# Kernel tuning notes

Hardware: AMD Instinct MI355X
Metric: run time of the kernel (lower is better)

The kernel has to match this reference:

```python
import jax, jax.numpy as jnp
import numpy as np
import math

BS = 32; N_NODE = 400; N = BS * N_NODE; E = 204800
D = 200; HS = 1024; SEQ = 512
N_NTYPE = 4; N_ETYPE = 38
HEADS = 4; DPH = D // HEADS
K_LAYERS = 5
EP1 = 1.0


def _lin(key, fi, fo, lead=None):
    shape = (fi, fo) if lead is None else (lead, fi, fo)
    return jax.random.normal(key, shape, jnp.float32) * 0.05


def setup_inputs() -> dict:
    key = jax.random.key(0)
    ks = jax.random.split(key, 20)
    inp = {}
    inp['hidden_states'] = jax.random.normal(ks[0], (BS, SEQ, HS), jnp.float32)
    inp['X'] = jax.random.normal(ks[1], (N, D), jnp.float32)
    inp['node_feature_extra'] = jax.random.normal(ks[2], (N, D), jnp.float32)
    inp['edge_index'] = jax.random.randint(ks[3], (2, E), 0, N)
    inp['edge_type'] = jax.random.randint(ks[4], (E,), 0, N_ETYPE)
    inp['node_type'] = jax.random.randint(ks[5], (N,), 0, N_NTYPE)
    inp['epoch'] = 0
    edge_in = N_ETYPE + 1 + 2 * N_NTYPE  # one-hot edge type (+self-loop) + head/tail node-type one-hots
    inp['We1'] = _lin(ks[6], edge_in, D); inp['be1'] = jnp.zeros((D,), jnp.float32)
    inp['We2'] = _lin(ks[7], D, D);       inp['be2'] = jnp.zeros((D,), jnp.float32)
    inp['Wkey'] = _lin(ks[8], 3 * D, D, K_LAYERS);  inp['bkey'] = jnp.zeros((K_LAYERS, D), jnp.float32)
    inp['Wmsg'] = _lin(ks[9], 3 * D, D, K_LAYERS);  inp['bmsg'] = jnp.zeros((K_LAYERS, D), jnp.float32)
    inp['Wqry'] = _lin(ks[10], 2 * D, D, K_LAYERS); inp['bqry'] = jnp.zeros((K_LAYERS, D), jnp.float32)
    inp['Wm1'] = _lin(ks[11], D, D, K_LAYERS);      inp['bm1'] = jnp.zeros((K_LAYERS, D), jnp.float32)
    inp['Wm2'] = _lin(ks[12], D, D, K_LAYERS);      inp['bm2'] = jnp.zeros((K_LAYERS, D), jnp.float32)
    inp['Wq_att'] = _lin(ks[13], D, D); inp['bq_att'] = jnp.zeros((D,), jnp.float32)
    inp['Wk_att'] = _lin(ks[14], D, D); inp['bk_att'] = jnp.zeros((D,), jnp.float32)
    inp['Wv_att'] = _lin(ks[15], D, D); inp['bv_att'] = jnp.zeros((D,), jnp.float32)
    inp['Wproj'] = _lin(ks[16], HS, D); inp['bproj'] = jnp.zeros((D,), jnp.float32)
    return inp


def _segment_softmax(scores, seg, n):
    m = jax.ops.segment_max(scores, seg, num_segments=n)
    m = jnp.where(jnp.isfinite(m), m, 0.0)
    e = jnp.exp(scores - m[seg])
    s = jax.ops.segment_sum(e, seg, num_segments=n)
    return e / (s[seg] + 1e-16)


def _gat_layer(X, nfe, src, dst, edge_emb, Wk, bk, Wm, bm, Wq, bq, W1, b1, W2, b2):
    n = X.shape[0]
    x = jnp.concatenate([X, nfe], axis=1)            # [N, 2D]
    x_i = x[dst]; x_j = x[src]                       # [E', 2D]
    key = (jnp.concatenate([x_i, edge_emb], 1) @ Wk + bk).reshape(-1, HEADS, DPH)
    msg = (jnp.concatenate([x_j, edge_emb], 1) @ Wm + bm).reshape(-1, HEADS, DPH)
    qry = ((x_i @ Wq + bq).reshape(-1, HEADS, DPH)) / math.sqrt(DPH)
    scores = (qry * key).sum(-1)                     # [E', HEADS]
    alpha = _segment_softmax(scores, src, n)
    cnt = jax.ops.segment_sum(jnp.ones_like(alpha[:, 0]), src, num_segments=n)[src]
    alpha = alpha * cnt[:, None]                     # scale by src out-degree (QAGNN GATConvE)
    out_msg = (msg * alpha[..., None]).reshape(-1, D)
    aggr = jax.ops.segment_sum(out_msg, dst, num_segments=n)
    out = jax.nn.relu(aggr @ W1 + b1) @ W2 + b2      # MLP, BatchNorm(eval) ~ identity
    sensitivity = jnp.max(jnp.linalg.norm(out, axis=-1))
    return out, sensitivity


def _forward(hidden_states, X, node_feature_extra, edge_index, edge_type, node_type,
             We1, be1, We2, be2, Wkey, bkey, Wmsg, bmsg, Wqry, bqry, Wm1, bm1, Wm2, bm2,
             Wq_att, bq_att, Wk_att, bk_att, Wv_att, bv_att, Wproj, bproj):
    n = X.shape[0]
    # self loops with edge type n_etype, as in GATConvE
    loop = jnp.arange(n)
    src = jnp.concatenate([edge_index[0], loop])
    dst = jnp.concatenate([edge_index[1], loop])
    et = jnp.concatenate([edge_type, jnp.full((n,), N_ETYPE, edge_type.dtype)])
    edge_vec = jax.nn.one_hot(et, N_ETYPE + 1, dtype=X.dtype)
    hvec = jax.nn.one_hot(node_type[src], N_NTYPE, dtype=X.dtype)
    tvec = jax.nn.one_hot(node_type[dst], N_NTYPE, dtype=X.dtype)
    # shared edge encoder (same edges each layer -> hoisted, identical math)
    edge_emb = jax.nn.relu(jnp.concatenate([edge_vec, hvec, tvec], 1) @ We1 + be1) @ We2 + be2
    context = hidden_states[:, 0, :] @ Wproj + bproj  # [bs, D]
    K = (context @ Wk_att + bk_att)[:, None, :]       # [bs, 1, D]
    V = (context @ Wv_att + bv_att)[:, None, :]
    nkey = jax.random.key(123)
    _X = X
    for li in range(K_LAYERS):
        _X, sens = _gat_layer(_X, node_feature_extra, src, dst, edge_emb,
                              Wkey[li], bkey[li], Wmsg[li], bmsg[li], Wqry[li], bqry[li],
                              Wm1[li], bm1[li], Wm2[li], bm2[li])
        _X = jax.nn.gelu(_X, approximate=False)
        Xb = _X.reshape(BS, N_NODE, D)
        Q = Xb @ Wq_att + bq_att
        Q = Q / jnp.maximum(jnp.linalg.norm(Q, axis=-1, keepdims=True), 1e-12)
        att = jnp.einsum('bnd,bmd->bnm', Q, K) / math.sqrt(D)  # [bs, n_node, 1]
        scale = jax.lax.stop_gradient(sens / (EP1 / 4.0))      # Laplace DP noise (non-diff in orig)
        noise = scale * jax.random.laplace(jax.random.fold_in(nkey, li), att.shape, att.dtype)
        att = att + noise
        _X = jnp.einsum('bnm,bmd->bnd', att, V).reshape(-1, D)
    return _X


def reference(hidden_states, X, node_feature_extra, edge_index, edge_type, node_type, epoch,
              We1, be1, We2, be2, Wkey, bkey, Wmsg, bmsg, Wqry, bqry, Wm1, bm1, Wm2, bm2,
              Wq_att, bq_att, Wk_att, bk_att, Wv_att, bv_att, Wproj, bproj):
    return _forward(hidden_states, X, node_feature_extra, edge_index, edge_type, node_type,
                    We1, be1, We2, be2, Wkey, bkey, Wmsg, bmsg, Wqry, bqry, Wm1, bm1, Wm2, bm2,
                    Wq_att, bq_att, Wk_att, bk_att, Wv_att, bv_att, Wproj, bproj)
```

## Files before the change

kernel.cpp:

```cpp
#include <hip/hip_runtime.h>
#include <stdint.h>

#define NBATCH 32
#define NNODE  400
#define NN     12800
#define NE     204800
#define EPE    217600
#define DD     200
#define NETYPE 38
#define NCOMBO 624
#define HSZ    1024
#define SEQQ   512
#define NL     5
#define ACH    128

__device__ __forceinline__ unsigned short f2bf(float x){
  uint32_t u = __float_as_uint(x);
  uint32_t r = (u + 0x7fffu + ((u>>16)&1u)) >> 16;
  return (unsigned short)r;
}
__device__ __forceinline__ float bf2f(unsigned short b){
  return __uint_as_float(((uint32_t)b)<<16);
}

__device__ __forceinline__ uint32_t rotl32(uint32_t x, uint32_t d){ return (x<<d)|(x>>(32u-d)); }

__device__ void tf2x32(uint32_t k0, uint32_t k1, uint32_t x0, uint32_t x1,
                       uint32_t* o0, uint32_t* o1){
  uint32_t ks0=k0, ks1=k1, ks2=k0^k1^0x1BD11BDAu;
  uint32_t ks[3]={ks0,ks1,ks2};
  x0 += ks0; x1 += ks1;
  const uint32_t rotA[4]={13,15,26,6};
  const uint32_t rotB[4]={17,29,16,24};
  #pragma unroll
  for (int i=0;i<5;i++){
    const uint32_t* r = (i&1)? rotB : rotA;
    #pragma unroll
    for (int j=0;j<4;j++){ x0 += x1; x1 = rotl32(x1, r[j]); x1 ^= x0; }
    x0 += ks[(i+1)%3];
    x1 += ks[(i+2)%3] + (uint32_t)(i+1);
  }
  *o0=x0; *o1=x1;
}

__global__ void k_noise(float* noise){
  int i = blockIdx.x*256+threadIdx.x;
  if (i >= NL*NN) return;
  int l = i / NN, j = i % NN;
  uint32_t k0,k1,o0,o1,bits;
  tf2x32(0u,123u,0u,(uint32_t)l,&k0,&k1);
  tf2x32(k0,k1,0u,(uint32_t)j,&o0,&o1);
  bits = o0 ^ o1;
  uint32_t fb = (bits>>9) | 0x3f800000u;
  float f = __uint_as_float(fb) - 1.0f;
  const float minv = -0.99999994039535522461f;
  float u = fmaxf(minv, f*2.0f + minv);
  float s = (u>0.f)?1.f:((u<0.f)?-1.f:0.f);
  noise[i] = s*log1pf(-fabsf(u));
}

__global__ void k_edges(const int* eidx, int* outdeg, int* indeg){
  int e = blockIdx.x*256+threadIdx.x; if (e>=EPE) return;
  int s,dv;
  if (e < NE){ s = eidx[e]; dv = eidx[NE+e]; } else { s = dv = e-NE; }
  atomicAdd(&outdeg[s],1); atomicAdd(&indeg[dv],1);
}

__global__ void k_scan(const int* outdeg, const int* indeg, int* sstart, int* dstart){
  __shared__ int buf[2][1024];
  for (int which=0; which<2; ++which){
    const int* a = which? indeg : outdeg;
    int* o = which? dstart : sstart;
    int t = threadIdx.x;
    int c0 = t*13;
    int s = 0;
    for (int i=c0;i<c0+13;i++) if (i<NN) s += a[i];
    __syncthreads();
    buf[0][t]=s; __syncthreads();
    int cur=0;
    #pragma unroll
    for (int off=1; off<1024; off<<=1){
      int v = buf[cur][t];
      if (t>=off) v += buf[cur][t-off];
      buf[cur^1][t]=v; cur^=1; __syncthreads();
    }
    int run = buf[cur][t] - s;
    for (int i=c0;i<c0+13;i++) if (i<NN){ o[i]=run; run+=a[i]; }
    if (t==0) o[NN]=EPE;
  }
}

__global__ void k_scatter(const int* eidx, const int* etype, const int* ntype,
                          const int* sstart, const int* dstart, int* sfill, int* dfill,
                          int* s_dst, int* s_combo, int* d_src, int* d_combo, int* s_dpos){
  int e = blockIdx.x*256+threadIdx.x; if (e>=EPE) return;
  int s,dv,et;
  if (e<NE){ s=eidx[e]; dv=eidx[NE+e]; et=etype[e]; } else { s=dv=e-NE; et=NETYPE; }
  int c = et*16 + ntype[s]*4 + ntype[dv];
  int p = sstart[s] + atomicAdd(&sfill[s],1);
  s_dst[p]=dv; s_combo[p]=c;
  int q = dstart[dv] + atomicAdd(&dfill[dv],1);
  d_src[q]=s; d_combo[q]=c; s_dpos[p]=q;
}

__global__ void k_ehid(const float* We1, const float* be1, float* ehid){
  int i = blockIdx.x*256+threadIdx.x; if (i>=NCOMBO*DD) return;
  int c = i/DD, d = i%DD;
  int et=c>>4, ht=(c>>2)&3, tt=c&3;
  float v = We1[et*DD+d] + We1[(39+ht)*DD+d] + We1[(43+tt)*DD+d] + be1[d];
  ehid[i] = fmaxf(v,0.f);
}

__global__ void k_cvt_xcat(const float* X, const float* nfe, unsigned short* xbf){
  int i=blockIdx.x*256+threadIdx.x; if (i>=NN*448) return;
  int n=i/448, d=i%448;
  float v = (d<200)? X[(size_t)n*200+d] : (d<400)? nfe[(size_t)n*200+(d-200)] : 0.f;
  xbf[i] = f2bf(v);
}
__global__ void k_cvt_nfe(const float* nfe, unsigned short* nbf){
  int i=blockIdx.x*256+threadIdx.x; if (i>=NN*224) return;
  int n=i/224, d=i%224;
  nbf[i] = (d<200)? f2bf(nfe[(size_t)n*200+d]) : 0;
}
__global__ void k_cvt_flat(const float* src, unsigned short* dst, int n){
  int i=blockIdx.x*256+threadIdx.x; if (i>=n) return;
  dst[i] = f2bf(src[i]);
}

struct WJob { const float* src; unsigned short* dst; int Ksrc; int Kpad; };
struct WArgs { WJob j[26]; };
__global__ void k_wswz(WArgs a){
  WJob jb = a.j[blockIdx.z];
  int i = blockIdx.x*256+threadIdx.x;
  if (i >= jb.Kpad*256) return;
  int k = i>>8, n = i&255;
  unsigned short v = 0;
  if (k<jb.Ksrc && n<200) v = f2bf(jb.src[(size_t)k*200+n]);
  jb.dst[(((size_t)(k>>3))*256 + n)*8 + (k&7)] = v;
}

typedef __attribute__((ext_vector_type(8))) short bf16x8;
typedef __attribute__((ext_vector_type(4))) float f32x4;

struct MJob { const unsigned short* A; const unsigned short* B; const float* bias;
              float* C; unsigned short* Cbf; const float* r1v; const float* r1m;
              int relu; float scale; int gelu; int cbfs; };
struct MArgs { int Kpad; MJob j[3]; };

__global__ __launch_bounds__(256) void k_mgemm(MArgs g){
  const MJob jb = g.j[blockIdx.z];
  const int lane = threadIdx.x&63, w = threadIdx.x>>6;
  const int lr = lane&15, lk = lane>>4;
  const int m0 = blockIdx.y*128 + w*32;
  const int n0 = blockIdx.x*64;
  const int Kp = g.Kpad;
  f32x4 acc[2][4] = {};
  const unsigned short* a0 = jb.A + (size_t)(m0+lr)*Kp + lk*8;
  const unsigned short* a1 = a0 + (size_t)16*Kp;
  for (int ks=0; ks<Kp; ks+=32){
    bf16x8 af0 = *(const bf16x8*)(a0 + ks);
    bf16x8 af1 = *(const bf16x8*)(a1 + ks);
    const unsigned short* bb = jb.B + (((size_t)(ks>>3) + lk)*256 + n0 + lr)*8;
    bf16x8 b0 = *(const bf16x8*)(bb);
    bf16x8 b1 = *(const bf16x8*)(bb + 128);
    bf16x8 b2 = *(const bf16x8*)(bb + 256);
    bf16x8 b3 = *(const bf16x8*)(bb + 384);
    acc[0][0]=__builtin_amdgcn_mfma_f32_16x16x32_bf16(af0,b0,acc[0][0],0,0,0);
    acc[0][1]=__builtin_amdgcn_mfma_f32_16x16x32_bf16(af0,b1,acc[0][1],0,0,0);
    acc[0][2]=__builtin_amdgcn_mfma_f32_16x16x32_bf16(af0,b2,acc[0][2],0,0,0);
    acc[0][3]=__builtin_amdgcn_mfma_f32_16x16x32_bf16(af0,b3,acc[0][3],0,0,0);
    acc[1][0]=__builtin_amdgcn_mfma_f32_16x16x32_bf16(af1,b0,acc[1][0],0,0,0);
    acc[1][1]=__builtin_amdgcn_mfma_f32_16x16x32_bf16(af1,b1,acc[1][1],0,0,0);
    acc[1][2]=__builtin_amdgcn_mfma_f32_16x16x32_bf16(af1,b2,acc[1][2],0,0,0);
    acc[1][3]=__builtin_amdgcn_mfma_f32_16x16x32_bf16(af1,b3,acc[1][3],0,0,0);
  }
  #pragma unroll
  for (int mt=0; mt<2; ++mt){
    int mbase = m0 + mt*16 + lk*4;
    #pragma unroll
    for (int nt=0; nt<4; ++nt){
      int n = n0 + nt*16 + lr;
      #pragma unroll
      for (int r=0;r<4;r++){
        int m = mbase + r;
        float v = acc[mt][nt][r];
        if (n < 200){
          if (jb.r1v)  v += jb.r1v[m]*jb.r1m[(size_t)(m/NNODE)*200 + n];
          if (jb.bias) v += jb.bias[n];
          v *= jb.scale;
          if (jb.relu) v = fmaxf(v, 0.f);
          if (jb.C)    jb.C[(size_t)m*200 + n] = v;
          if (jb.Cbf){
            float o = jb.gelu? 0.5f*v*(1.0f+erff(v*0.70710678118654752440f)) : v;
            jb.Cbf[(size_t)m*jb.cbfs + n] = f2bf(o);
          }
        } else if (jb.Cbf && jb.cbfs==224 && n < 224){
          jb.Cbf[(size_t)m*224 + n] = 0;
        }
      }
    }
  }
}

struct RJob { const float* A; const float* W; const float* bias; float* C; int K; size_t lda; };
struct RArgs { RJob j[12]; float* part; int NS; int Kc; };
__global__ __launch_bounds__(256) void k_rowpart(RArgs a){
  RJob jb = a.j[blockIdx.z];
  int m = blockIdx.x, s = blockIdx.y;
  int k0 = s*a.Kc, k1 = k0 + a.Kc; if (k1 > jb.K) k1 = jb.K;
  int kc = k1 - k0;
  __shared__ float row[128];
  const float* ap = jb.A + (size_t)m*jb.lda + k0;
  for (int k=threadIdx.x; k<kc; k+=256) row[k]=ap[k];
  __syncthreads();
  int n = threadIdx.x;
  if (n < 200){
    float acc = 0.f;
    const float* wp = jb.W + (size_t)k0*200 + n;
    for (int kk=0; kk<kc; ++kk) acc += row[kk]*wp[(size_t)kk*200];
    a.part[(((size_t)blockIdx.z*32 + m)*8 + s)*200 + n] = acc;
  }
}
__global__ __launch_bounds__(256) void k_rowred(RArgs a){
  RJob jb = a.j[blockIdx.z];
  int m = blockIdx.x, n = threadIdx.x;
  if (n >= 200) return;
  float acc = jb.bias? jb.bias[n] : 0.f;
  for (int s=0; s<a.NS; ++s) acc += a.part[(((size_t)blockIdx.z*32 + m)*8 + s)*200 + n];
  jb.C[(size_t)m*200+n] = acc;
}

struct Job {
  const float* A; const float* W; const float* bias; float* C;
  const float* r1v; const float* r1m; int relu;
};
struct GArgs { int M,N,K,lda; Job j[12]; };

#define BMT 64
#define BNT 64
#define BKT 16

__global__ __launch_bounds__(256) void k_gemm(GArgs g){
  const Job jb = g.j[blockIdx.z];
  const int m0 = blockIdx.y*BMT, n0 = blockIdx.x*BNT;
  __shared__ float As[BKT][BMT+4];
  __shared__ float Bs[BKT][BNT+4];
  float acc[4][4]={};
  const int t = threadIdx.x;
  const int tx = t & 15, ty = t >> 4;
  for (int k0=0; k0<g.K; k0+=BKT){
    {
      int r = t>>2, cq = t&3;
      int m = m0+r, k = k0+cq*4;
      float4 v = make_float4(0.f,0.f,0.f,0.f);
      if (m < g.M && k < g.K){
        if (k+3 < g.K) v = *(const float4*)(jb.A + (size_t)m*g.lda + k);
        else {
          const float* ap = jb.A + (size_t)m*g.lda;
          float tm[4]={0.f,0.f,0.f,0.f};
          for (int qq=0;qq<4;qq++) if (k+qq<g.K) tm[qq]=ap[k+qq];
          v = make_float4(tm[0],tm[1],tm[2],tm[3]);
        }
      }
      As[cq*4+0][r]=v.x; As[cq*4+1][r]=v.y; As[cq*4+2][r]=v.z; As[cq*4+3][r]=v.w;
    }
    {
      int r = t>>4, cq = t&15;
      int k = k0+r, n = n0+cq*4;
      float4 v = make_float4(0.f,0.f,0.f,0.f);
      if (k < g.K && n < g.N){
        if (n+3 < g.N) v = *(const float4*)(jb.W + (size_t)k*g.N + n);
        else { const float* wp = jb.W + (size_t)k*g.N;
          float tm[4]={0.f,0.f,0.f,0.f};
          for (int qq=0;qq<4;qq++) if (n+qq<g.N) tm[qq]=wp[n+qq];
          v = make_float4(tm[0],tm[1],tm[2],tm[3]); }
      }
      Bs[r][cq*4+0]=v.x; Bs[r][cq*4+1]=v.y; Bs[r][cq*4+2]=v.z; Bs[r][cq*4+3]=v.w;
    }
    __syncthreads();
    int kend = g.K-k0; if (kend>BKT) kend=BKT;
    for (int kk=0;kk<kend;kk++){
      float4 av = *(const float4*)&As[kk][ty*4];
      float4 bv = *(const float4*)&Bs[kk][tx*4];
      float a[4]={av.x,av.y,av.z,av.w};
      float b[4]={bv.x,bv.y,bv.z,bv.w};
      #pragma unroll
      for (int i=0;i<4;i++){
        #pragma unroll
        for (int jq=0;jq<4;jq++) acc[i][jq] += a[i]*b[jq];
      }
    }
    __syncthreads();
  }
  #pragma unroll
  for (int i=0;i<4;i++){
    int m = m0+ty*4+i; if (m>=g.M) continue;
    int bidx = m / NNODE;
    #pragma unroll
    for (int jq=0;jq<4;jq++){
      int n = n0+tx*4+jq; if (n>=g.N) continue;
      float v = acc[i][jq];
      if (jb.bias) v += jb.bias[n];
      if (jb.r1v)  v += jb.r1v[m]*jb.r1m[(size_t)bidx*g.N + n];
      if (jb.relu) v = fmaxf(v,0.f);
      jb.C[(size_t)m*g.N+n] = v;
    }
  }
}

__global__ void k_prep(const float* qv, const float* Ak, float* ps){
  int wid = threadIdx.x>>6, lane = threadIdx.x&63;
  int n = blockIdx.x*4 + wid; if (n>=NN) return;
  float acch[4]={0.f,0.f,0.f,0.f};
  for (int d=lane; d<DD; d+=64)
    acch[d/50] += qv[(size_t)n*DD+d]*Ak[(size_t)n*DD+d];
  for (int off=1; off<64; off<<=1){
    #pragma unroll
    for (int h=0;h<4;h++) acch[h] += __shfl_xor(acch[h], off);
  }
  if (lane==0){
    #pragma unroll
    for (int h=0;h<4;h++) ps[n*4+h]=acch[h];
  }
}

__global__ __launch_bounds__(256) void k_score(const int* s_dst, const int* s_combo, const float* qv,
                        const float* Bk, const float* ps, float* scores){
  int p = blockIdx.x*64 + (threadIdx.x>>2);
  if (p>=EPE) return;
  int sub = threadIdx.x&3;
  int dv = s_dst[p], c = s_combo[p];
  const float4* qr = (const float4*)(qv + (size_t)dv*DD);
  const float4* br = (const float4*)(Bk + (size_t)c*DD);
  float acc[4]={0.f,0.f,0.f,0.f};
  #pragma unroll
  for (int i=0;i<13;i++){
    int q = sub + 4*i;
    if (q < 50){
      float4 a = qr[q], b = br[q];
      int d = q*4;
      acc[(d+0)/50] += a.x*b.x;
      acc[(d+1)/50] += a.y*b.y;
      acc[(d+2)/50] += a.z*b.z;
      acc[(d+3)/50] += a.w*b.w;
    }
  }
  #pragma unroll
  for (int off=1; off<4; off<<=1){
    #pragma unroll
    for (int h=0;h<4;h++) acc[h] += __shfl_xor(acc[h], off);
  }
  scores[(size_t)p*4+sub] = ps[dv*4+sub] + acc[sub];
}

__global__ void k_softmax(const int* sstart, const int* s_dpos, const float* scores, float* alpha_d){
  int n = blockIdx.x;
  int st = sstart[n], en = sstart[n+1];
  int cnt = en-st;
  int t = threadIdx.x;
  float mx = -3.402823466e38f;
  for (int i=t; i<cnt*4; i+=64) mx = fmaxf(mx, scores[(size_t)(st+(i>>2))*4 + (i&3)]);
  for (int off=4; off<64; off<<=1) mx = fmaxf(mx, __shfl_xor(mx,off));
  float sm=0.f;
  for (int i=t; i<cnt*4; i+=64) sm += expf(scores[(size_t)(st+(i>>2))*4 + (i&3)] - mx);
  for (int off=4; off<64; off<<=1) sm += __shfl_xor(sm,off);
  float scale = (float)cnt / (sm + 1e-16f);
  for (int i=t; i<cnt*4; i+=64){
    int p = st+(i>>2), h = i&3;
    float a = expf(scores[(size_t)p*4+h]-mx)*scale;
    alpha_d[(size_t)s_dpos[p]*4+h] = a;
  }
}

__global__ __launch_bounds__(256) void k_aggr(const int* dstart, const int* d_src, const int* d_combo,
                       const float* alpha_d,
                       const unsigned short* Am, const unsigned short* Bm,
                       unsigned short* aggr_bf){
  __shared__ float red[4][200];
  __shared__ float s_al[ACH*4];
  __shared__ int   s_s[ACH], s_c[ACH];
  int v = blockIdx.x;
  int w = threadIdx.x>>6, lane = threadIdx.x&63;
  int st=dstart[v], en=dstart[v+1];
  float acc[8]={0.f,0.f,0.f,0.f,0.f,0.f,0.f,0.f};
  int h[8];
  #pragma unroll
  for (int j=0;j<8;j++) h[j] = (lane*8+j)/50;
  for (int c0=st; c0<en; c0+=ACH){
    int cnt = en-c0; if (cnt>ACH) cnt=ACH;
    __syncthreads();
    for (int i=threadIdx.x; i<cnt; i+=256){ s_s[i]=d_src[c0+i]; s_c[i]=d_combo[c0+i]; }
    for (int i=threadIdx.x; i<cnt*4; i+=256){ s_al[i]=alpha_d[(size_t)c0*4+i]; }
    __syncthreads();
    if (lane < 25){
      for (int q=w; q<cnt; q+=4){
        int s=s_s[q], c=s_c[q];
        bf16x8 am = *(const bf16x8*)(Am + (size_t)s*200 + lane*8);
        bf16x8 bm = *(const bf16x8*)(Bm + (size_t)c*200 + lane*8);
        #pragma unroll
        for (int j=0;j<8;j++){
          float a = s_al[q*4+h[j]];
          acc[j] += a*(bf2f((unsigned short)am[j]) + bf2f((unsigned short)bm[j]));
        }
      }
    }
  }
  if (lane < 25){
    #pragma unroll
    for (int j=0;j<8;j++) red[w][lane*8+j]=acc[j];
  }
  __syncthreads();
  int d = threadIdx.x;
  if (d < 200){
    float r = red[0][d]+red[1][d]+red[2][d]+red[3][d];
    aggr_bf[(size_t)v*224+d]=f2bf(r);
  } else if (d < 224){
    aggr_bf[(size_t)v*224+d]=0;
  }
}

__global__ void k_sens(const float* out, float* sens2, int l){
  __shared__ float smax[4];
  int wid = threadIdx.x>>6, lane = threadIdx.x&63;
  int gw = blockIdx.x*4 + wid;
  float mx = 0.f;
  for (int n = gw; n < NN; n += 256){
    const float4* row = (const float4*)(out + (size_t)n*DD);
    float ss = 0.f;
    if (lane < 50){ float4 v = row[lane]; ss = v.x*v.x + v.y*v.y + v.z*v.z + v.w*v.w; }
    for (int off=1; off<64; off<<=1) ss += __shfl_xor(ss, off);
    mx = fmaxf(mx, ss);
  }
  if (lane==0) smax[wid] = mx;
  __syncthreads();
  if (threadIdx.x==0){
    float m = fmaxf(fmaxf(smax[0],smax[1]),fmaxf(smax[2],smax[3]));
    atomicMax((int*)&sens2[l], __float_as_int(m));
  }
}

__global__ void k_att(const float* Q, const float* Katt, const float* Vatt,
                      const float* sens2, const float* noise, int l,
                      float* att, float* outX){
  int wid=threadIdx.x>>6, lane=threadIdx.x&63;
  int n=blockIdx.x*4+wid; if (n>=NN) return;
  int b=n/NNODE;
  float qq=0.f, qk=0.f;
  for (int d=lane; d<DD; d+=64){
    float q=Q[(size_t)n*DD+d];
    qq += q*q; qk += q*Katt[b*DD+d];
  }
  for (int off=1;off<64;off<<=1){ qq+=__shfl_xor(qq,off); qk+=__shfl_xor(qk,off); }
  float nrm = fmaxf(sqrtf(qq), 1e-12f);
  float a = (qk/nrm) * 0.07071067811865475244f;
  a += 4.0f*sqrtf(sens2[l]) * noise[(size_t)l*NN + n];
  if (lane==0) att[n]=a;
  if (outX){
    for (int d=lane; d<DD; d+=64) outX[(size_t)n*DD+d] = a*Vatt[b*DD+d];
  }
}

static inline Job mkjob(const float* A, const float* W, const float* bias, float* C,
                        const float* r1v, const float* r1m, int relu){
  Job j; j.A=A; j.W=W; j.bias=bias; j.C=C; j.r1v=r1v; j.r1m=r1m; j.relu=relu; return j;
}

static inline void gemm_launch(hipStream_t stream, int M,int N,int K,int lda,
                               const Job* jobs, int nj){
  GArgs g; g.M=M; g.N=N; g.K=K; g.lda=lda;
  for (int i=0;i<nj;i++) g.j[i]=jobs[i];
  for (int i=nj;i<12;i++) g.j[i]=jobs[0];
  dim3 grid((N+BNT-1)/BNT,(M+BMT-1)/BMT,nj);
  k_gemm<<<grid,256,0,stream>>>(g);
}

static inline RJob mkrjob(const float* A, const float* W, const float* bias, float* C,
                          int K, size_t lda){
  RJob j; j.A=A; j.W=W; j.bias=bias; j.C=C; j.K=K; j.lda=lda; return j;
}

static inline void rgemm_launch(hipStream_t stream, const RJob* jobs, int nj,
                                float* part, int NS, int Kc){
  RArgs a;
  for (int i=0;i<nj;i++) a.j[i]=jobs[i];
  for (int i=nj;i<12;i++) a.j[i]=jobs[0];
  a.part = part; a.NS = NS; a.Kc = Kc;
  k_rowpart<<<dim3(NBATCH,NS,nj),256,0,stream>>>(a);
  k_rowred <<<dim3(NBATCH,1,nj),256,0,stream>>>(a);
}

static inline MJob mkmjob(const unsigned short* A, const unsigned short* B, const float* bias,
                          float* C, unsigned short* Cbf, const float* r1v, const float* r1m,
                          int relu, float scale, int gelu, int cbfs){
  MJob j; j.A=A; j.B=B; j.bias=bias; j.C=C; j.Cbf=Cbf; j.r1v=r1v; j.r1m=r1m;
  j.relu=relu; j.scale=scale; j.gelu=gelu; j.cbfs=cbfs; return j;
}

static inline void mgemm_launch(hipStream_t stream, int Kpad, const MJob* jobs, int nj){
  MArgs a; a.Kpad=Kpad;
  for (int i=0;i<nj;i++) a.j[i]=jobs[i];
  for (int i=nj;i<3;i++) a.j[i]=jobs[0];
  k_mgemm<<<dim3(4,100,nj),256,0,stream>>>(a);
}

extern "C" void kernel_launch(void* const* d_in, const int* in_sizes, int n_in,
                              void* d_out, int out_size, void* d_ws, size_t ws_size,
                              hipStream_t stream){
  const float* hs    = (const float*)d_in[0];
  const float* X     = (const float*)d_in[1];
  const float* nfe   = (const float*)d_in[2];
  const int*   eidx  = (const int*)d_in[3];
  const int*   etype = (const int*)d_in[4];
  const int*   ntype = (const int*)d_in[5];
  const float* We1   = (const float*)d_in[7];
  const float* be1   = (const float*)d_in[8];
  const float* We2   = (const float*)d_in[9];
  const float* be2   = (const float*)d_in[10];
  const float* Wkey  = (const float*)d_in[11];
  const float* bkey  = (const float*)d_in[12];
  const float* Wmsg  = (const float*)d_in[13];
  const float* bmsg  = (const float*)d_in[14];
  const float* Wqry  = (const float*)d_in[15];
  const float* bqry  = (const float*)d_in[16];
  const float* Wm1   = (const float*)d_in[17];
  const float* bm1   = (const float*)d_in[18];
  const float* Wm2   = (const float*)d_in[19];
  const float* bm2   = (const float*)d_in[20];
  const float* Wq_att= (const float*)d_in[21];
  const float* bq_att= (const float*)d_in[22];
  const float* Wk_att= (const float*)d_in[23];
  const float* bk_att= (const float*)d_in[24];
  const float* Wv_att= (const float*)d_in[25];
  const float* bv_att= (const float*)d_in[26];
  const float* Wproj = (const float*)d_in[27];
  const float* bproj = (const float*)d_in[28];
  float* outp = (float*)d_out;

  char* cur = (char*)d_ws;
  auto allocf = [&](size_t n)->float*{ float* p=(float*)cur; cur += ((n*4+255)/256)*256; return p; };
  auto alloci = [&](size_t n)->int*  { int*   p=(int*)cur;   cur += ((n*4+255)/256)*256; return p; };
  auto allocb = [&](size_t n)->unsigned short*{ unsigned short* p=(unsigned short*)cur; cur += ((n*2+255)/256)*256; return p; };

  float* noise  = allocf((size_t)NL*NN);
  float* ehid   = allocf((size_t)NCOMBO*DD);
  float* eemb   = allocf((size_t)NCOMBO*DD);
  float* Bk     = allocf((size_t)NL*NCOMBO*DD);
  float* Bm     = allocf((size_t)NL*NCOMBO*DD);
  float* context= allocf((size_t)NBATCH*DD);
  float* Katt   = allocf((size_t)NBATCH*DD);
  float* Vatt   = allocf((size_t)NBATCH*DD);
  float* CKk    = allocf((size_t)4*NBATCH*DD);
  float* CKm    = allocf((size_t)4*NBATCH*DD);
  float* CKq    = allocf((size_t)4*NBATCH*DD);
  float* Ak     = allocf((size_t)NN*DD);
  float* Aq     = allocf((size_t)NN*DD);
  float* ps     = allocf((size_t)NN*4);
  float* scores = allocf((size_t)EPE*4);
  float* alphad = allocf((size_t)EPE*4);
  float* Q      = allocf((size_t)NN*DD);
  float* outb   = allocf((size_t)NN*DD);
  float* att    = allocf((size_t)NN);
  float* sens2  = allocf(8);
  float* rpart  = allocf((size_t)12*NBATCH*8*200);
  unsigned short* am_bf   = allocb((size_t)NN*200);
  unsigned short* bm_bf   = allocb((size_t)NL*NCOMBO*DD);
  unsigned short* xcat_bf = allocb((size_t)NN*448);
  unsigned short* nfe_bf  = allocb((size_t)NN*224);
  unsigned short* aggr_bf = allocb((size_t)NN*224);
  unsigned short* tmp1_bf = allocb((size_t)NN*224);
  unsigned short* gelu_bf = allocb((size_t)NN*224);
  unsigned short* wkx0  = allocb((size_t)448*256);
  unsigned short* wmx0  = allocb((size_t)448*256);
  unsigned short* wqx0  = allocb((size_t)448*256);
  unsigned short* wkN   = allocb((size_t)4*224*256);
  unsigned short* wmN   = allocb((size_t)4*224*256);
  unsigned short* wqN   = allocb((size_t)4*224*256);
  unsigned short* wm1s  = allocb((size_t)5*224*256);
  unsigned short* wm2s  = allocb((size_t)5*224*256);
  unsigned short* wqatts= allocb((size_t)224*256);
  int* sstart = alloci(NN+1);
  int* dstart = alloci(NN+1);
  int* outdeg = alloci(NN);
  int* indeg  = alloci(NN);
  int* sfill  = alloci(NN);
  int* dfill  = alloci(NN);
  int* s_dst  = alloci(EPE);
  int* s_combo= alloci(EPE);
  int* d_src  = alloci(EPE);
  int* d_combo= alloci(EPE);
  int* s_dpos = alloci(EPE);
  if ((size_t)(cur-(char*)d_ws) > ws_size) return;

  hipMemsetAsync(outdeg,0,(size_t)4*NN*4,stream);
  hipMemsetAsync(sens2 ,0,32,stream);

  k_noise<<<(NL*NN+255)/256,256,0,stream>>>(noise);
  k_edges<<<(EPE+255)/256,256,0,stream>>>(eidx,outdeg,indeg);
  k_scan<<<1,1024,0,stream>>>(outdeg,indeg,sstart,dstart);
  k_scatter<<<(EPE+255)/256,256,0,stream>>>(eidx,etype,ntype,sstart,dstart,sfill,dfill,
                                            s_dst,s_combo,d_src,d_combo,s_dpos);
  k_ehid<<<(NCOMBO*DD+255)/256,256,0,stream>>>(We1,be1,ehid);
  { Job j = mkjob(ehid,We2,be2,eemb,0,0,0); gemm_launch(stream,NCOMBO,DD,DD,DD,&j,1); }
  { Job js[10];
    for (int l=0;l<NL;l++){
      js[2*l+0]=mkjob(eemb, Wkey + (size_t)l*600*DD + 400*DD, 0, Bk + (size_t)l*NCOMBO*DD, 0,0,0);
      js[2*l+1]=mkjob(eemb, Wmsg + (size_t)l*600*DD + 400*DD, bmsg + (size_t)l*DD,
                      Bm + (size_t)l*NCOMBO*DD, 0,0,0);
    }
    gemm_launch(stream,NCOMBO,DD,DD,DD,js,10);
  }
  k_cvt_flat<<<(NL*NCOMBO*DD+255)/256,256,0,stream>>>(Bm, bm_bf, NL*NCOMBO*DD);
  k_cvt_xcat<<<(NN*448+255)/256,256,0,stream>>>(X,nfe,xcat_bf);
  k_cvt_nfe<<<(NN*224+255)/256,256,0,stream>>>(nfe,nfe_bf);
  { WArgs wa; int wn=0;
    auto addw=[&](const float* s, unsigned short* d, int Ks, int Kp){
      wa.j[wn].src=s; wa.j[wn].dst=d; wa.j[wn].Ksrc=Ks; wa.j[wn].Kpad=Kp; wn++; };
    addw(Wkey, wkx0, 400,448);
    addw(Wmsg, wmx0, 400,448);
    addw(Wqry, wqx0, 400,448);
    for (int l=1;l<NL;l++){
      addw(Wkey + (size_t)l*600*DD + 200*DD, wkN + (size_t)(l-1)*224*256, 200,224);
      addw(Wmsg + (size_t)l*600*DD + 200*DD, wmN + (size_t)(l-1)*224*256, 200,224);
      addw(Wqry + (size_t)l*400*DD + 200*DD, wqN + (size_t)(l-1)*224*256, 200,224);
    }
    for (int l=0;l<NL;l++){
      addw(Wm1 + (size_t)l*DD*DD, wm1s + (size_t)l*224*256, 200,224);
      addw(Wm2 + (size_t)l*DD*DD, wm2s + (size_t)l*224*256, 200,224);
    }
    addw(Wq_att, wqatts, 200,224);
    k_wswz<<<dim3(448,1,wn),256,0,stream>>>(wa);
  }
  { RJob j = mkrjob(hs, Wproj, bproj, context, HSZ, (size_t)SEQQ*HSZ);
    rgemm_launch(stream, &j, 1, rpart, 8, 128); }
  { RJob js[2] = { mkrjob(context, Wk_att, bk_att, Katt, DD, DD),
                   mkrjob(context, Wv_att, bv_att, Vatt, DD, DD) };
    rgemm_launch(stream, js, 2, rpart, 2, 100); }
  { RJob js[12];
    for (int l=1;l<NL;l++){
      js[3*(l-1)+0]=mkrjob(Vatt, Wkey + (size_t)l*600*DD, 0, CKk + (size_t)(l-1)*NBATCH*DD, DD, DD);
      js[3*(l-1)+1]=mkrjob(Vatt, Wmsg + (size_t)l*600*DD, 0, CKm + (size_t)(l-1)*NBATCH*DD, DD, DD);
      js[3*(l-1)+2]=mkrjob(Vatt, Wqry + (size_t)l*400*DD, 0, CKq + (size_t)(l-1)*NBATCH*DD, DD, DD);
    }
    rgemm_launch(stream, js, 12, rpart, 4, 50);
  }

  const float invs = 0.14142135623730950488f;
  for (int l=0;l<NL;l++){
    const float* bkey_l = bkey + (size_t)l*DD;
    const float* bqry_l = bqry + (size_t)l*DD;
    const float* Bk_l = Bk + (size_t)l*NCOMBO*DD;
    const unsigned short* Bm_l = bm_bf + (size_t)l*NCOMBO*DD;

    if (l==0){
      MJob js[3] = { mkmjob(xcat_bf, wkx0, bkey_l, Ak, 0,     0,0,0, 1.f,0, 224),
                     mkmjob(xcat_bf, wmx0, 0,      0,  am_bf, 0,0,0, 1.f,0, 200),
                     mkmjob(xcat_bf, wqx0, bqry_l, Aq, 0,     0,0,0, invs,0, 224) };
      mgemm_launch(stream,448,js,3);
    } else {
      const float* ckk = CKk + (size_t)(l-1)*NBATCH*DD;
      const float* ckm = CKm + (size_t)(l-1)*NBATCH*DD;
      const float* ckq = CKq + (size_t)(l-1)*NBATCH*DD;
      MJob js[3] = { mkmjob(nfe_bf, wkN + (size_t)(l-1)*224*256, bkey_l, Ak, 0,     att, ckk, 0, 1.f,0, 224),
                     mkmjob(nfe_bf, wmN + (size_t)(l-1)*224*256, 0,      0,  am_bf, att, ckm, 0, 1.f,0, 200),
                     mkmjob(nfe_bf, wqN + (size_t)(l-1)*224*256, bqry_l, Aq, 0,     att, ckq, 0, invs,0, 224) };
      mgemm_launch(stream,224,js,3);
    }
    k_prep<<<NN/4,256,0,stream>>>(Aq,Ak,ps);
    k_score<<<(EPE*4+255)/256,256,0,stream>>>(s_dst,s_combo,Aq,Bk_l,ps,scores);
    k_softmax<<<NN,64,0,stream>>>(sstart,s_dpos,scores,alphad);
    k_aggr<<<NN,256,0,stream>>>(dstart,d_src,d_combo,alphad,am_bf,Bm_l,aggr_bf);
    { MJob j = mkmjob(aggr_bf, wm1s + (size_t)l*224*256, bm1 + (size_t)l*DD, 0, tmp1_bf, 0,0,1, 1.f,0, 224);
      mgemm_launch(stream,224,&j,1); }
    { MJob j = mkmjob(tmp1_bf, wm2s + (size_t)l*224*256, bm2 + (size_t)l*DD, outb, gelu_bf, 0,0,0, 1.f,1, 224);
      mgemm_launch(stream,224,&j,1); }
    k_sens<<<64,256,0,stream>>>(outb,sens2,l);
    { MJob j = mkmjob(gelu_bf, wqatts, bq_att, Q, 0, 0,0,0, 1.f,0, 224);
      mgemm_launch(stream,224,&j,1); }
    k_att<<<NN/4,256,0,stream>>>(Q,Katt,Vatt,sens2,noise,l,att,(l==NL-1)? outp : (float*)0);
  }
}
```

Measured before the change: 1.119 ms.

## Fuse key/query/message GEMMs with per-head query-key dot product

Replaces the three-job batched GEMM plus the separate k_prep kernel with one kernel that computes key, query and message projections per 64-row block and reduces the query·key per-head dot products in registers. This removes the fp32 Ak buffer write and re-read, and drops a kernel launch. In exchange the grid shrinks to 200 blocks, each doing all three GEMMs serially over all 256 output columns with no LDS tiling, so there is less parallelism on the GPU and the A fragments are reloaded per pass.

```diff
diff --git a/kernel.cpp b/kernel.cpp
--- a/kernel.cpp
+++ b/kernel.cpp
@@ -141,6 +141,113 @@
 
 typedef __attribute__((ext_vector_type(8))) short bf16x8;
 typedef __attribute__((ext_vector_type(4))) float f32x4;
+
+struct M3Args {
+  const unsigned short* A; int Kp;
+  const unsigned short *wk, *wq, *wm;
+  const float *bkey, *bqry;
+  const float *att, *ckk, *ckq, *ckm;
+  float* qv; unsigned short* am; float* ps; float invs;
+};
+
+__device__ __forceinline__ void mm16(const unsigned short* a0, const unsigned short* W,
+                                     int Kp, int n0, int lk, int lr, f32x4 acc[4]){
+  for (int ks=0; ks<Kp; ks+=32){
+    bf16x8 af = *(const bf16x8*)(a0 + ks);
+    const unsigned short* bb = W + (((size_t)(ks>>3)+lk)*256 + n0 + lr)*8;
+    acc[0]=__builtin_amdgcn_mfma_f32_16x16x32_bf16(af, *(const bf16x8*)(bb      ), acc[0],0,0,0);
+    acc[1]=__builtin_amdgcn_mfma_f32_16x16x32_bf16(af, *(const bf16x8*)(bb + 128), acc[1],0,0,0);
+    acc[2]=__builtin_amdgcn_mfma_f32_16x16x32_bf16(af, *(const bf16x8*)(bb + 256), acc[2],0,0,0);
+    acc[3]=__builtin_amdgcn_mfma_f32_16x16x32_bf16(af, *(const bf16x8*)(bb + 384), acc[3],0,0,0);
+  }
+}
+
+__global__ __launch_bounds__(256) void k_mgemm3(M3Args g){
+  const int lane = threadIdx.x&63, w = threadIdx.x>>6;
+  const int lr = lane&15, lk = lane>>4;
+  const int mw = blockIdx.x*64 + w*16;
+  const int Kp = g.Kp;
+  const unsigned short* a0 = g.A + (size_t)(mw+lr)*Kp + lk*8;
+
+  int   mrow[4]; int bidx[4]; float attv[4];
+  #pragma unroll
+  for (int rr=0;rr<4;rr++){
+    mrow[rr] = mw + lk*4 + rr;
+    bidx[rr] = mrow[rr]/NNODE;
+    attv[rr] = g.att ? g.att[mrow[rr]] : 0.f;
+  }
+  float ps[4][4] = {};
+  float akv[4][4];
+
+  #pragma unroll
+  for (int ni=0; ni<4; ++ni){
+    const int n0 = ni*64;
+    {
+      f32x4 acc[4] = {};
+      mm16(a0, g.wk, Kp, n0, lk, lr, acc);
+      #pragma unroll
+      for (int nt=0;nt<4;nt++){
+        int d = n0 + nt*16 + lr;
+        bool ok = d < 200;
+        float bias = ok? g.bkey[d] : 0.f;
+        #pragma unroll
+        for (int rr=0;rr<4;rr++){
+          float v = acc[nt][rr] + bias;
+          if (g.att && ok) v += attv[rr]*g.ckk[(size_t)bidx[rr]*200 + d];
+          akv[nt][rr] = ok? v : 0.f;
+        }
+      }
+    }
+    {
+      f32x4 acc[4] = {};
+      mm16(a0, g.wq, Kp, n0, lk, lr, acc);
+      #pragma unroll
+      for (int nt=0;nt<4;nt++){
+        int d = n0 + nt*16 + lr;
+        bool ok = d < 200;
+        float bias = ok? g.bqry[d] : 0.f;
+        int hd = d/50;
+        #pragma unroll
+        for (int rr=0;rr<4;rr++){
+          float v = acc[nt][rr] + bias;
+          if (g.att && ok) v += attv[rr]*g.ckq[(size_t)bidx[rr]*200 + d];
+          v *= g.invs;
+          if (ok){
+            g.qv[(size_t)mrow[rr]*200 + d] = v;
+            float p = v*akv[nt][rr];
+            #pragma unroll
+            for (int h=0;h<4;h++) ps[rr][h] += (hd==h)? p : 0.f;
+          }
+        }
+      }
+    }
+    {
+      f32x4 acc[4] = {};
+      mm16(a0, g.wm, Kp, n0, lk, lr, acc);
+      #pragma unroll
+      for (int nt=0;nt<4;nt++){
+        int d = n0 + nt*16 + lr;
+        bool ok = d < 200;
+        #pragma unroll
+        for (int rr=0;rr<4;rr++){
+          float v = acc[nt][rr];
+          if (g.att && ok) v += attv[rr]*g.ckm[(size_t)bidx[rr]*200 + d];
+          if (ok) g.am[(size_t)mrow[rr]*200 + d] = f2bf(v);
+        }
+      }
+    }
+  }
+  #pragma unroll
+  for (int rr=0;rr<4;rr++){
+    #pragma unroll
+    for (int h=0;h<4;h++){
+      float v = ps[rr][h];
+      v += __shfl_xor(v,1); v += __shfl_xor(v,2);
+      v += __shfl_xor(v,4); v += __shfl_xor(v,8);
+      if (lr==0) g.ps[(size_t)mrow[rr]*4 + h] = v;
+    }
+  }
+}
 
 struct MJob { const unsigned short* A; const unsigned short* B; const float* bias;
               float* C; unsigned short* Cbf; const float* r1v; const float* r1m;
@@ -305,22 +412,6 @@
       if (jb.relu) v = fmaxf(v,0.f);
       jb.C[(size_t)m*g.N+n] = v;
     }
-  }
-}
-
-__global__ void k_prep(const float* qv, const float* Ak, float* ps){
-  int wid = threadIdx.x>>6, lane = threadIdx.x&63;
-  int n = blockIdx.x*4 + wid; if (n>=NN) return;
-  float acch[4]={0.f,0.f,0.f,0.f};
-  for (int d=lane; d<DD; d+=64)
-    acch[d/50] += qv[(size_t)n*DD+d]*Ak[(size_t)n*DD+d];
-  for (int off=1; off<64; off<<=1){
-    #pragma unroll
-    for (int h=0;h<4;h++) acch[h] += __shfl_xor(acch[h], off);
-  }
-  if (lane==0){
-    #pragma unroll
-    for (int h=0;h<4;h++) ps[n*4+h]=acch[h];
   }
 }
 
@@ -552,7 +643,6 @@
   float* CKk    = allocf((size_t)4*NBATCH*DD);
   float* CKm    = allocf((size_t)4*NBATCH*DD);
   float* CKq    = allocf((size_t)4*NBATCH*DD);
-  float* Ak     = allocf((size_t)NN*DD);
   float* Aq     = allocf((size_t)NN*DD);
   float* ps     = allocf((size_t)NN*4);
   float* scores = allocf((size_t)EPE*4);
@@ -651,21 +741,24 @@
     const float* Bk_l = Bk + (size_t)l*NCOMBO*DD;
     const unsigned short* Bm_l = bm_bf + (size_t)l*NCOMBO*DD;
 
-    if (l==0){
-      MJob js[3] = { mkmjob(xcat_bf, wkx0, bkey_l, Ak, 0,     0,0,0, 1.f,0, 224),
-                     mkmjob(xcat_bf, wmx0, 0,      0,  am_bf, 0,0,0, 1.f,0, 200),
-                     mkmjob(xcat_bf, wqx0, bqry_l, Aq, 0,     0,0,0, invs,0, 224) };
-      mgemm_launch(stream,448,js,3);
-    } else {
-      const float* ckk = CKk + (size_t)(l-1)*NBATCH*DD;
-      const float* ckm = CKm + (size_t)(l-1)*NBATCH*DD;
-      const float* ckq = CKq + (size_t)(l-1)*NBATCH*DD;
-      MJob js[3] = { mkmjob(nfe_bf, wkN + (size_t)(l-1)*224*256, bkey_l, Ak, 0,     att, ckk, 0, 1.f,0, 224),
-                     mkmjob(nfe_bf, wmN + (size_t)(l-1)*224*256, 0,      0,  am_bf, att, ckm, 0, 1.f,0, 200),
-                     mkmjob(nfe_bf, wqN + (size_t)(l-1)*224*256, bqry_l, Aq, 0,     att, ckq, 0, invs,0, 224) };
-      mgemm_launch(stream,224,js,3);
-    }
-    k_prep<<<NN/4,256,0,stream>>>(Aq,Ak,ps);
+    { M3Args a;
+      if (l==0){
+        a.A = xcat_bf; a.Kp = 448; a.wk = wkx0; a.wq = wqx0; a.wm = wmx0;
+        a.att = 0; a.ckk = 0; a.ckq = 0; a.ckm = 0;
+      } else {
+        a.A = nfe_bf; a.Kp = 224;
+        a.wk = wkN + (size_t)(l-1)*224*256;
+        a.wq = wqN + (size_t)(l-1)*224*256;
+        a.wm = wmN + (size_t)(l-1)*224*256;
+        a.att = att;
+        a.ckk = CKk + (size_t)(l-1)*NBATCH*DD;
+        a.ckq = CKq + (size_t)(l-1)*NBATCH*DD;
+        a.ckm = CKm + (size_t)(l-1)*NBATCH*DD;
+      }
+      a.bkey = bkey_l; a.bqry = bqry_l;
+      a.qv = Aq; a.am = am_bf; a.ps = ps; a.invs = invs;
+      k_mgemm3<<<200,256,0,stream>>>(a);
+    }
     k_score<<<(EPE*4+255)/256,256,0,stream>>>(s_dst,s_combo,Aq,Bk_l,ps,scores);
     k_softmax<<<NN,64,0,stream>>>(sstart,s_dpos,scores,alphad);
     k_aggr<<<NN,256,0,stream>>>(dstart,d_src,d_combo,alphad,am_bf,Bm_l,aggr_bf);
```

After: 1.291 ms. 15.4% more time.

## Store query/key/Q activations and key combo table in bf16 for scoring

Applied to the files above, without the earlier changes.

The GEMMs producing Ak, Aq and the attention Q now write bf16 outputs instead of fp32. The key-side combo table Bk is also converted to bf16 once. k_prep, k_score and k_att are rewritten to read 16-byte bf16x8 vectors, which halves the gather traffic in the edge-scoring kernel. This trades accuracy of the attention scores and the Q normalisation for lower memory bandwidth. It also adds an extra conversion pass over Bk.

```diff
diff --git a/kernel.cpp b/kernel.cpp
--- a/kernel.cpp
+++ b/kernel.cpp
@@ -308,12 +308,22 @@
   }
 }
 
-__global__ void k_prep(const float* qv, const float* Ak, float* ps){
+__global__ void k_prep(const unsigned short* qv, const unsigned short* ak, float* ps){
   int wid = threadIdx.x>>6, lane = threadIdx.x&63;
   int n = blockIdx.x*4 + wid; if (n>=NN) return;
   float acch[4]={0.f,0.f,0.f,0.f};
-  for (int d=lane; d<DD; d+=64)
-    acch[d/50] += qv[(size_t)n*DD+d]*Ak[(size_t)n*DD+d];
+  if (lane < 25){
+    bf16x8 q = *(const bf16x8*)(qv + (size_t)n*200 + lane*8);
+    bf16x8 a = *(const bf16x8*)(ak + (size_t)n*200 + lane*8);
+    #pragma unroll
+    for (int j=0;j<8;j++){
+      int d = lane*8+j;
+      int hd = (d>=50)+(d>=100)+(d>=150);
+      float p = bf2f((unsigned short)q[j])*bf2f((unsigned short)a[j]);
+      #pragma unroll
+      for (int h=0;h<4;h++) acch[h] += (hd==h)? p : 0.f;
+    }
+  }
   for (int off=1; off<64; off<<=1){
     #pragma unroll
     for (int h=0;h<4;h++) acch[h] += __shfl_xor(acch[h], off);
@@ -324,25 +334,30 @@
   }
 }
 
-__global__ __launch_bounds__(256) void k_score(const int* s_dst, const int* s_combo, const float* qv,
-                        const float* Bk, const float* ps, float* scores){
+__global__ __launch_bounds__(256) void k_score(const int* s_dst, const int* s_combo,
+                        const unsigned short* qv, const unsigned short* Bk,
+                        const float* ps, float* scores){
   int p = blockIdx.x*64 + (threadIdx.x>>2);
   if (p>=EPE) return;
   int sub = threadIdx.x&3;
   int dv = s_dst[p], c = s_combo[p];
-  const float4* qr = (const float4*)(qv + (size_t)dv*DD);
-  const float4* br = (const float4*)(Bk + (size_t)c*DD);
+  const unsigned short* qr = qv + (size_t)dv*200;
+  const unsigned short* br = Bk + (size_t)c*200;
   float acc[4]={0.f,0.f,0.f,0.f};
   #pragma unroll
-  for (int i=0;i<13;i++){
-    int q = sub + 4*i;
-    if (q < 50){
-      float4 a = qr[q], b = br[q];
-      int d = q*4;
-      acc[(d+0)/50] += a.x*b.x;
-      acc[(d+1)/50] += a.y*b.y;
-      acc[(d+2)/50] += a.z*b.z;
-      acc[(d+3)/50] += a.w*b.w;
+  for (int i=0;i<7;i++){
+    int ch = sub + 4*i;
+    if (ch < 25){
+      bf16x8 q = *(const bf16x8*)(qr + ch*8);
+      bf16x8 b = *(const bf16x8*)(br + ch*8);
+      #pragma unroll
+      for (int j=0;j<8;j++){
+        int d = ch*8+j;
+        int hd = (d>=50)+(d>=100)+(d>=150);
+        float pr = bf2f((unsigned short)q[j])*bf2f((unsigned short)b[j]);
+        #pragma unroll
+        for (int h=0;h<4;h++) acc[h] += (hd==h)? pr : 0.f;
+      }
     }
   }
   #pragma unroll
@@ -439,7 +454,7 @@
   }
 }
 
-__global__ void k_att(const float* Q, const float* Katt, const float* Vatt,
+__global__ void k_att(const unsigned short* Qb, const float* Katt, const float* Vatt,
                       const float* sens2, const float* noise, int l,
                       float* att, float* outX){
   int wid=threadIdx.x>>6, lane=threadIdx.x&63;
@@ -447,7 +462,7 @@
   int b=n/NNODE;
   float qq=0.f, qk=0.f;
   for (int d=lane; d<DD; d+=64){
-    float q=Q[(size_t)n*DD+d];
+    float q=bf2f(Qb[(size_t)n*200+d]);
     qq += q*q; qk += q*Katt[b*DD+d];
   }
   for (int off=1;off<64;off<<=1){ qq+=__shfl_xor(qq,off); qk+=__shfl_xor(qk,off); }
@@ -552,18 +567,19 @@
   float* CKk    = allocf((size_t)4*NBATCH*DD);
   float* CKm    = allocf((size_t)4*NBATCH*DD);
   float* CKq    = allocf((size_t)4*NBATCH*DD);
-  float* Ak     = allocf((size_t)NN*DD);
-  float* Aq     = allocf((size_t)NN*DD);
   float* ps     = allocf((size_t)NN*4);
   float* scores = allocf((size_t)EPE*4);
   float* alphad = allocf((size_t)EPE*4);
-  float* Q      = allocf((size_t)NN*DD);
   float* outb   = allocf((size_t)NN*DD);
   float* att    = allocf((size_t)NN);
   float* sens2  = allocf(8);
   float* rpart  = allocf((size_t)12*NBATCH*8*200);
+  unsigned short* ak_bf   = allocb((size_t)NN*200);
+  unsigned short* qv_bf   = allocb((size_t)NN*200);
+  unsigned short* q_bf    = allocb((size_t)NN*200);
   unsigned short* am_bf   = allocb((size_t)NN*200);
   unsigned short* bm_bf   = allocb((size_t)NL*NCOMBO*DD);
+  unsigned short* bk_bf   = allocb((size_t)NL*NCOMBO*DD);
   unsigned short* xcat_bf = allocb((size_t)NN*448);
   unsigned short* nfe_bf  = allocb((size_t)NN*224);
   unsigned short* aggr_bf = allocb((size_t)NN*224);
@@ -610,6 +626,7 @@
     gemm_launch(stream,NCOMBO,DD,DD,DD,js,10);
   }
   k_cvt_flat<<<(NL*NCOMBO*DD+255)/256,256,0,stream>>>(Bm, bm_bf, NL*NCOMBO*DD);
+  k_cvt_flat<<<(NL*NCOMBO*DD+255)/256,256,0,stream>>>(Bk, bk_bf, NL*NCOMBO*DD);
   k_cvt_xcat<<<(NN*448+255)/256,256,0,stream>>>(X,nfe,xcat_bf);
   k_cvt_nfe<<<(NN*224+255)/256,256,0,stream>>>(nfe,nfe_bf);
   { WArgs wa; int wn=0;
@@ -648,25 +665,25 @@
   for (int l=0;l<NL;l++){
     const float* bkey_l = bkey + (size_t)l*DD;
     const float* bqry_l = bqry + (size_t)l*DD;
-    const float* Bk_l = Bk + (size_t)l*NCOMBO*DD;
+    const unsigned short* Bk_l = bk_bf + (size_t)l*NCOMBO*DD;
     const unsigned short* Bm_l = bm_bf + (size_t)l*NCOMBO*DD;
 
     if (l==0){
-      MJob js[3] = { mkmjob(xcat_bf, wkx0, bkey_l, Ak, 0,     0,0,0, 1.f,0, 224),
-                     mkmjob(xcat_bf, wmx0, 0,      0,  am_bf, 0,0,0, 1.f,0, 200),
-                     mkmjob(xcat_bf, wqx0, bqry_l, Aq, 0,     0,0,0, invs,0, 224) };
+      MJob js[3] = { mkmjob(xcat_bf, wkx0, bkey_l, 0, ak_bf, 0,0,0, 1.f,0, 200),
+                     mkmjob(xcat_bf, wmx0, 0,      0, am_bf, 0,0,0, 1.f,0, 200),
+                     mkmjob(xcat_bf, wqx0, bqry_l, 0, qv_bf, 0,0,0, invs,0, 200) };
       mgemm_launch(stream,448,js,3);
     } else {
       const float* ckk = CKk + (size_t)(l-1)*NBATCH*DD;
       const float* ckm = CKm + (size_t)(l-1)*NBATCH*DD;
       const float* ckq = CKq + (size_t)(l-1)*NBATCH*DD;
-      MJob js[3] = { mkmjob(nfe_bf, wkN + (size_t)(l-1)*224*256, bkey_l, Ak, 0,     att, ckk, 0, 1.f,0, 224),
-                     mkmjob(nfe_bf, wmN + (size_t)(l-1)*224*256, 0,      0,  am_bf, att, ckm, 0, 1.f,0, 200),
-                     mkmjob(nfe_bf, wqN + (size_t)(l-1)*224*256, bqry_l, Aq, 0,     att, ckq, 0, invs,0, 224) };
+      MJob js[3] = { mkmjob(nfe_bf, wkN + (size_t)(l-1)*224*256, bkey_l, 0, ak_bf, att, ckk, 0, 1.f,0, 200),
+                     mkmjob(nfe_bf, wmN + (size_t)(l-1)*224*256, 0,      0, am_bf, att, ckm, 0, 1.f,0, 200),
+                     mkmjob(nfe_bf, wqN + (size_t)(l-1)*224*256, bqry_l, 0, qv_bf, att, ckq, 0, invs,0, 200) };
       mgemm_launch(stream,224,js,3);
     }
-    k_prep<<<NN/4,256,0,stream>>>(Aq,Ak,ps);
-    k_score<<<(EPE*4+255)/256,256,0,stream>>>(s_dst,s_combo,Aq,Bk_l,ps,scores);
+    k_prep<<<NN/4,256,0,stream>>>(qv_bf,ak_bf,ps);
+    k_score<<<(EPE*4+255)/256,256,0,stream>>>(s_dst,s_combo,qv_bf,Bk_l,ps,scores);
     k_softmax<<<NN,64,0,stream>>>(sstart,s_dpos,scores,alphad);
     k_aggr<<<NN,256,0,stream>>>(dstart,d_src,d_combo,alphad,am_bf,Bm_l,aggr_bf);
     { MJob j = mkmjob(aggr_bf, wm1s + (size_t)l*224*256, bm1 + (size_t)l*DD, 0, tmp1_bf, 0,0,1, 1.f,0, 224);
@@ -674,8 +691,8 @@
     { MJob j = mkmjob(tmp1_bf, wm2s + (size_t)l*224*256, bm2 + (size_t)l*DD, outb, gelu_bf, 0,0,0, 1.f,1, 224);
       mgemm_launch(stream,224,&j,1); }
     k_sens<<<64,256,0,stream>>>(outb,sens2,l);
-    { MJob j = mkmjob(gelu_bf, wqatts, bq_att, Q, 0, 0,0,0, 1.f,0, 224);
+    { MJob j = mkmjob(gelu_bf, wqatts, bq_att, 0, q_bf, 0,0,0, 1.f,0, 200);
       mgemm_launch(stream,224,&j,1); }
-    k_att<<<NN/4,256,0,stream>>>(Q,Katt,Vatt,sens2,noise,l,att,(l==NL-1)? outp : (float*)0);
-  }
-}
+    k_att<<<NN/4,256,0,stream>>>(q_bf,Katt,Vatt,sens2,noise,l,att,(l==NL-1)? outp : (float*)0);
+  }
+}
```

Measured after the change: 1.043 ms. 6.8% less time.
